# Kernel optimization log

Measured on AMD Instinct MI355X. Metric: run time of the kernel, lower is better.

Reference implementation:

```python
import jax, jax.numpy as jnp
import numpy as np

INPUT_DIM, CB_DIM, CB_VOCAB = 512, 16, 8192
N = 16384
EPS = 1e-12  # F.normalize default eps


def setup_inputs() -> dict:
    key = jax.random.key(0)
    kx, kp, kc = jax.random.split(key, 3)
    x = jax.random.normal(kx, (N, INPUT_DIM), dtype=jnp.float32)
    # xavier_uniform_ on P [input_dim, cb_dim]
    bound = float(np.sqrt(6.0 / (INPUT_DIM + CB_DIM)))
    P = jax.random.uniform(kp, (INPUT_DIM, CB_DIM), dtype=jnp.float32,
                           minval=-bound, maxval=bound)
    # CB = F.normalize(randn(cb_vocab, cb_dim)) -> unit rows
    CB = jax.random.normal(kc, (CB_VOCAB, CB_DIM), dtype=jnp.float32)
    CB = CB / jnp.maximum(jnp.linalg.norm(CB, axis=1, keepdims=True), EPS)
    return {"x": x, "P": P, "CB": CB}


def reference(x, P, CB):
    # random projection: [N, input_dim] @ [input_dim, cb_dim] -> [N, cb_dim]
    xp = x @ P
    # L2-normalize projected vectors (rows)
    xp = xp / jnp.maximum(jnp.linalg.norm(xp, axis=1, keepdims=True), EPS)
    # cosine similarity against unit-norm codebook = plain dot product
    sim = xp @ CB.T  # [N, cb_vocab]
    return jnp.argmax(sim, axis=1)  # [N] int codebook indices
```

## Files before the change

kernel.cpp:

```cpp
#include <hip/hip_runtime.h>
#include <stdint.h>

#define N_ROWS   16384
#define IN_DIM   512
#define CB_DIM   16
#define CB_VOCAB 8192

#define PROJ_ROWS 128
#define PROJ_GROUPS (N_ROWS / PROJ_ROWS)
#define KSPLIT 4
#define PROJ_BLOCKS (PROJ_GROUPS * KSPLIT)

#define N_RT   (N_ROWS / 16)
#define N_CT   (CB_VOCAB / 16)
#define CODEPARTS 16
#define CT_PER_PART (N_CT / CODEPARTS)

#define WS_OFF_XPP   0
#define WS_OFF_AFA   (4u << 20)
#define WS_OFF_AFB   (5u << 20)
#define WS_OFF_BHH   (6u << 20)
#define WS_OFF_B31   ((6u << 20) + (512u << 10))
#define WS_OFF_PART  (7u << 20)

typedef __attribute__((ext_vector_type(8))) short bf16x8;
typedef __attribute__((ext_vector_type(4))) float f32x4;

__device__ __forceinline__ unsigned fkey(float f) {
    unsigned u = __float_as_uint(f);
    return (u & 0x80000000u) ? ~u : (u | 0x80000000u);
}

__device__ __forceinline__ unsigned short f2bf(float f) {
    unsigned u = __float_as_uint(f);
    return (unsigned short)((u + 0x7FFFu + ((u >> 16) & 1u)) >> 16);
}
__device__ __forceinline__ float bf2f(unsigned short h) {
    return __uint_as_float(((unsigned)h) << 16);
}

__global__ __launch_bounds__(256, 4)
void k_front(const float* __restrict__ x, const float* __restrict__ P,
             const float* __restrict__ CB, float* __restrict__ xp_part,
             bf16x8* __restrict__ Bhh, bf16x8* __restrict__ B31) {
    __shared__ float4 Ps[128 * 4];
    __shared__ float  accs[4][128][17];

    const int wave = threadIdx.x >> 6;
    const int lane = threadIdx.x & 63;

    if (blockIdx.x >= PROJ_BLOCKS) {
        const int ct   = (blockIdx.x - PROJ_BLOCKS) * 4 + wave;
        const int n    = lane & 15;
        const int quad = lane >> 4;
        const int kh   = (quad & 1) * 8;
        const int lvl  = quad >> 1;
        const int code = ct * 16 + n;

        const float4* b4 = (const float4*)(CB + (size_t)code * CB_DIM + kh);
        float4 a = b4[0], b = b4[1];
        float v[8] = {a.x, a.y, a.z, a.w, b.x, b.y, b.z, b.w};

        bf16x8 shh, s31;
#pragma unroll
        for (int j = 0; j < 8; ++j) {
            float f = v[j];
            unsigned short b1 = f2bf(f);  float r1 = f - bf2f(b1);
            unsigned short b2 = f2bf(r1); float r2 = r1 - bf2f(b2);
            unsigned short b3 = f2bf(r2);
            shh[j] = (short)(lvl ? b2 : b1);
            s31[j] = (short)(lvl ? b1 : b3);
        }
        Bhh[(size_t)ct * 64 + lane] = shh;
        B31[(size_t)ct * 64 + lane] = s31;
        return;
    }

    const int g = blockIdx.x >> 2;
    const int p = blockIdx.x & 3;

    for (int i = threadIdx.x; i < 512; i += 256)
        Ps[i] = ((const float4*)P)[p * 512 + i];
    __syncthreads();

    const int row0 = PROJ_ROWS * g + 2 * lane;
    const int kabs = 128 * p + 32 * wave;

    float acc0[16], acc1[16];
#pragma unroll
    for (int c = 0; c < 16; ++c) { acc0[c] = 0.f; acc1[c] = 0.f; }

    const float4* xr0 = (const float4*)(x + (size_t)row0 * IN_DIM + kabs);
    const float4* xr1 = (const float4*)(x + (size_t)(row0 + 1) * IN_DIM + kabs);

#pragma unroll
    for (int i = 0; i < 8; ++i) {
        float4 xa = xr0[i];
        float4 xb = xr1[i];
        float xas[4] = {xa.x, xa.y, xa.z, xa.w};
        float xbs[4] = {xb.x, xb.y, xb.z, xb.w};
#pragma unroll
        for (int kk = 0; kk < 4; ++kk) {
#pragma unroll
            for (int q = 0; q < 4; ++q) {
                float4 pv = Ps[(32 * wave + 4 * i + kk) * 4 + q];
                acc0[4 * q + 0] += xas[kk] * pv.x;
                acc0[4 * q + 1] += xas[kk] * pv.y;
                acc0[4 * q + 2] += xas[kk] * pv.z;
                acc0[4 * q + 3] += xas[kk] * pv.w;
                acc1[4 * q + 0] += xbs[kk] * pv.x;
                acc1[4 * q + 1] += xbs[kk] * pv.y;
                acc1[4 * q + 2] += xbs[kk] * pv.z;
                acc1[4 * q + 3] += xbs[kk] * pv.w;
            }
        }
    }

#pragma unroll
    for (int c = 0; c < 16; ++c) {
        accs[wave][2 * lane][c]     = acc0[c];
        accs[wave][2 * lane + 1][c] = acc1[c];
    }
    __syncthreads();

    float4* xpp = (float4*)xp_part;
#pragma unroll
    for (int it = 0; it < 2; ++it) {
        int idx = threadIdx.x + 256 * it;
        int r = idx >> 2, q = idx & 3;
        float4 s = {0.f, 0.f, 0.f, 0.f};
#pragma unroll
        for (int w = 0; w < 4; ++w) {
            s.x += accs[w][r][4 * q + 0];
            s.y += accs[w][r][4 * q + 1];
            s.z += accs[w][r][4 * q + 2];
            s.w += accs[w][r][4 * q + 3];
        }
        xpp[(size_t)p * (N_ROWS * 4) + (size_t)(PROJ_ROWS * g + r) * 4 + q] = s;
    }
}

__global__ __launch_bounds__(256, 4)
void k_fold_frag(const float* __restrict__ xp_part,
                 bf16x8* __restrict__ AfragA, bf16x8* __restrict__ AfragB) {
    const int wave = threadIdx.x >> 6;
    const int lane = threadIdx.x & 63;
    const int rt   = blockIdx.x * 4 + wave;
    const int m    = lane & 15;
    const int quad = lane >> 4;
    const int kh   = (quad & 1) * 8;
    const int lvl  = quad >> 1;
    const int row  = rt * 16 + m;

    const float* base = xp_part + (size_t)row * 16 + kh;
    float4 u0 = {0.f,0.f,0.f,0.f}, u1 = {0.f,0.f,0.f,0.f};
#pragma unroll
    for (int p = 0; p < 4; ++p) {
        const float4* b4 = (const float4*)(base + (size_t)p * (N_ROWS * 16));
        float4 a = b4[0], b = b4[1];
        u0.x += a.x; u0.y += a.y; u0.z += a.z; u0.w += a.w;
        u1.x += b.x; u1.y += b.y; u1.z += b.z; u1.w += b.w;
    }
    float v[8] = {u0.x, u0.y, u0.z, u0.w, u1.x, u1.y, u1.z, u1.w};

    bf16x8 sa, sb;
#pragma unroll
    for (int j = 0; j < 8; ++j) {
        float f = v[j];
        unsigned short b1 = f2bf(f);  float r1 = f - bf2f(b1);
        unsigned short b2 = f2bf(r1); float r2 = r1 - bf2f(b2);
        unsigned short b3 = f2bf(r2);
        sa[j] = (short)(lvl ? b2 : b1);
        sb[j] = (short)(lvl ? b3 : b1);
    }
    AfragA[(size_t)rt * 64 + lane] = sa;
    AfragB[(size_t)rt * 64 + lane] = sb;
}

__global__ __launch_bounds__(256, 4)
void k_scan(const bf16x8* __restrict__ AfragA, const bf16x8* __restrict__ AfragB,
            const bf16x8* __restrict__ Bhh, const bf16x8* __restrict__ B31,
            unsigned long long* __restrict__ part) {
    const int codepart = blockIdx.x & (CODEPARTS - 1);
    const int rowgrp   = blockIdx.x >> 4;
    const int wave     = threadIdx.x >> 6;
    const int lane     = threadIdx.x & 63;
    const int n        = lane & 15;
    const int quad     = lane >> 4;
    const int rt_base  = rowgrp * 16 + wave * 4;

    bf16x8 Aa[4], Ab[4];
#pragma unroll
    for (int t = 0; t < 4; ++t) {
        Aa[t] = AfragA[(size_t)(rt_base + t) * 64 + lane];
        Ab[t] = AfragB[(size_t)(rt_base + t) * 64 + lane];
    }

    float bestv[4][4];
    int   bestc[4][4];
#pragma unroll
    for (int t = 0; t < 4; ++t)
#pragma unroll
        for (int r = 0; r < 4; ++r) { bestv[t][r] = -INFINITY; bestc[t][r] = 0; }

    const int ct0 = codepart * CT_PER_PART;
    size_t ib = (size_t)ct0 * 64;
    bf16x8 nb1  = Bhh[ib + lane];
    bf16x8 nb1s = Bhh[ib + (lane ^ 32)];
    bf16x8 nb3  = B31[ib + lane];

    for (int c = 0; c < CT_PER_PART; ++c) {
        bf16x8 b1 = nb1, b1s = nb1s, b3 = nb3;
        if (c + 1 < CT_PER_PART) {
            size_t ibn = (size_t)(ct0 + c + 1) * 64;
            nb1  = Bhh[ibn + lane];
            nb1s = Bhh[ibn + (lane ^ 32)];
            nb3  = B31[ibn + lane];
        }
#pragma unroll
        for (int t = 0; t < 4; ++t) {
            f32x4 s = __builtin_amdgcn_mfma_f32_16x16x32_bf16(
                          Aa[t], b1, (f32x4){0.f, 0.f, 0.f, 0.f}, 0, 0, 0);
            s = __builtin_amdgcn_mfma_f32_16x16x32_bf16(Aa[t], b1s, s, 0, 0, 0);
            s = __builtin_amdgcn_mfma_f32_16x16x32_bf16(Ab[t], b3,  s, 0, 0, 0);
#pragma unroll
            for (int r = 0; r < 4; ++r) {
                if (s[r] > bestv[t][r]) { bestv[t][r] = s[r]; bestc[t][r] = c; }
            }
        }
    }

#pragma unroll
    for (int t = 0; t < 4; ++t) {
#pragma unroll
        for (int r = 0; r < 4; ++r) {
            unsigned code = (unsigned)(codepart * 512 + bestc[t][r] * 16 + n);
            unsigned long long packed =
                ((unsigned long long)fkey(bestv[t][r]) << 32) |
                (unsigned long long)(0xFFFFFFFFu - code);
#pragma unroll
            for (int mk = 1; mk <= 8; mk <<= 1) {
                unsigned long long o = __shfl_xor(packed, mk, 64);
                packed = (o > packed) ? o : packed;
            }
            if (n == 0) {
                int row = (rt_base + t) * 16 + quad * 4 + r;
                part[(size_t)codepart * N_ROWS + row] = packed;
            }
        }
    }
}

__global__ __launch_bounds__(256, 4)
void k_reduce(const unsigned long long* __restrict__ part,
              int* __restrict__ out) {
    int row = blockIdx.x * 256 + threadIdx.x;
    unsigned long long best = 0ull;
#pragma unroll
    for (int c = 0; c < CODEPARTS; ++c) {
        unsigned long long v = part[(size_t)c * N_ROWS + row];
        best = (v > best) ? v : best;
    }
    out[row] = (int)(0xFFFFFFFFu - (unsigned)(best & 0xFFFFFFFFull));
}

extern "C" void kernel_launch(void* const* d_in, const int* in_sizes, int n_in,
                              void* d_out, int out_size, void* d_ws, size_t ws_size,
                              hipStream_t stream) {
    const float* x  = (const float*)d_in[0];
    const float* P  = (const float*)d_in[1];
    const float* CB = (const float*)d_in[2];
    int* out = (int*)d_out;

    char* ws = (char*)d_ws;
    float*  xp_part = (float*)(ws + WS_OFF_XPP);
    bf16x8* AfragA  = (bf16x8*)(ws + WS_OFF_AFA);
    bf16x8* AfragB  = (bf16x8*)(ws + WS_OFF_AFB);
    bf16x8* Bhh     = (bf16x8*)(ws + WS_OFF_BHH);
    bf16x8* B31     = (bf16x8*)(ws + WS_OFF_B31);
    unsigned long long* part = (unsigned long long*)(ws + WS_OFF_PART);

    k_front<<<PROJ_BLOCKS + N_CT / 4, 256, 0, stream>>>(x, P, CB, xp_part,
                                                        Bhh, B31);
    k_fold_frag<<<N_RT / 4, 256, 0, stream>>>(xp_part, AfragA, AfragB);
    k_scan<<<(N_RT / 16) * CODEPARTS, 256, 0, stream>>>(AfragA, AfragB,
                                                        Bhh, B31, part);
    k_reduce<<<N_ROWS / 256, 256, 0, stream>>>(part, out);
}
```

Baseline: 113.9 us.

## Fuse projection with fragment packing and fold argmax reduction into scan via atomics

The projection kernel now handles 32 full rows per block. It reduces the K-split partial sums in shared memory and emits the bf16 split fragments directly, which removes the separate fold kernel and the xp_part global round trip. The final argmax reduction kernel is also removed. The scan does a 64-bit atomicMax into a per-row slot, and the last block per row group, found with an atomic counter, writes the output indices. This cuts the launch count from four to two and drops the intermediate traffic, at the cost of atomic contention and lower occupancy in the front kernel (launch bounds go from 4 to 2).

Result: no change. 113.7 us (median of 2 runs) (-0.2%).

```diff
diff --git a/kernel.cpp b/kernel.cpp
--- a/kernel.cpp
+++ b/kernel.cpp
@@ -6,22 +6,21 @@
 #define CB_DIM   16
 #define CB_VOCAB 8192
 
-#define PROJ_ROWS 128
-#define PROJ_GROUPS (N_ROWS / PROJ_ROWS)
-#define KSPLIT 4
-#define PROJ_BLOCKS (PROJ_GROUPS * KSPLIT)
+#define PROJ_BLOCKS 512
+#define PREP_BLOCKS 128
 
 #define N_RT   (N_ROWS / 16)
 #define N_CT   (CB_VOCAB / 16)
 #define CODEPARTS 16
 #define CT_PER_PART (N_CT / CODEPARTS)
-
-#define WS_OFF_XPP   0
-#define WS_OFF_AFA   (4u << 20)
-#define WS_OFF_AFB   (5u << 20)
-#define WS_OFF_BHH   (6u << 20)
-#define WS_OFF_B31   ((6u << 20) + (512u << 10))
-#define WS_OFF_PART  (7u << 20)
+#define N_ROWGRP 64
+
+#define WS_OFF_AFA  0
+#define WS_OFF_AFB  (1u << 20)
+#define WS_OFF_BHH  (2u << 20)
+#define WS_OFF_B31  ((2u << 20) + (512u << 10))
+#define WS_OFF_PART (3u << 20)
+#define WS_OFF_CNT  ((3u << 20) + (128u << 10))
 
 typedef __attribute__((ext_vector_type(8))) short bf16x8;
 typedef __attribute__((ext_vector_type(4))) float f32x4;
@@ -39,18 +38,24 @@
     return __uint_as_float(((unsigned)h) << 16);
 }
 
-__global__ __launch_bounds__(256, 4)
+__global__ __launch_bounds__(256, 2)
 void k_front(const float* __restrict__ x, const float* __restrict__ P,
-             const float* __restrict__ CB, float* __restrict__ xp_part,
-             bf16x8* __restrict__ Bhh, bf16x8* __restrict__ B31) {
-    __shared__ float4 Ps[128 * 4];
-    __shared__ float  accs[4][128][17];
+             const float* __restrict__ CB,
+             bf16x8* __restrict__ AfragA, bf16x8* __restrict__ AfragB,
+             bf16x8* __restrict__ Bhh, bf16x8* __restrict__ B31,
+             unsigned long long* __restrict__ part, unsigned* __restrict__ cnt) {
+    __shared__ float4 Ps[IN_DIM * 4];
+    __shared__ float  accs[8][32][20];
 
     const int wave = threadIdx.x >> 6;
     const int lane = threadIdx.x & 63;
 
     if (blockIdx.x >= PROJ_BLOCKS) {
-        const int ct   = (blockIdx.x - PROJ_BLOCKS) * 4 + wave;
+        const int pb = blockIdx.x - PROJ_BLOCKS;
+        if (threadIdx.x < 128) part[pb * 128 + threadIdx.x] = 0ull;
+        if (pb == 0 && threadIdx.x < 64) cnt[threadIdx.x] = 0u;
+
+        const int ct   = pb * 4 + wave;
         const int n    = lane & 15;
         const int quad = lane >> 4;
         const int kh   = (quad & 1) * 8;
@@ -76,111 +81,83 @@
         return;
     }
 
-    const int g = blockIdx.x >> 2;
-    const int p = blockIdx.x & 3;
-
-    for (int i = threadIdx.x; i < 512; i += 256)
-        Ps[i] = ((const float4*)P)[p * 512 + i];
-    __syncthreads();
-
-    const int row0 = PROJ_ROWS * g + 2 * lane;
-    const int kabs = 128 * p + 32 * wave;
-
-    float acc0[16], acc1[16];
-#pragma unroll
-    for (int c = 0; c < 16; ++c) { acc0[c] = 0.f; acc1[c] = 0.f; }
-
-    const float4* xr0 = (const float4*)(x + (size_t)row0 * IN_DIM + kabs);
-    const float4* xr1 = (const float4*)(x + (size_t)(row0 + 1) * IN_DIM + kabs);
-
-#pragma unroll
-    for (int i = 0; i < 8; ++i) {
-        float4 xa = xr0[i];
-        float4 xb = xr1[i];
-        float xas[4] = {xa.x, xa.y, xa.z, xa.w};
-        float xbs[4] = {xb.x, xb.y, xb.z, xb.w};
+    const int b = blockIdx.x;
+    for (int i = threadIdx.x; i < IN_DIM * 4; i += 256)
+        Ps[i] = ((const float4*)P)[i];
+    __syncthreads();
+
+    const int r32   = lane & 31;
+    const int khalf = lane >> 5;
+    const int row   = b * 32 + r32;
+    const int kb    = 128 * wave + 64 * khalf;
+
+    float acc[16];
+#pragma unroll
+    for (int c = 0; c < 16; ++c) acc[c] = 0.0f;
+
+    const float4* xr = (const float4*)(x + (size_t)row * IN_DIM + kb);
+
+#pragma unroll 4
+    for (int i = 0; i < 16; ++i) {
+        float4 xv = xr[i];
+        float xs[4] = {xv.x, xv.y, xv.z, xv.w};
 #pragma unroll
         for (int kk = 0; kk < 4; ++kk) {
 #pragma unroll
             for (int q = 0; q < 4; ++q) {
-                float4 pv = Ps[(32 * wave + 4 * i + kk) * 4 + q];
-                acc0[4 * q + 0] += xas[kk] * pv.x;
-                acc0[4 * q + 1] += xas[kk] * pv.y;
-                acc0[4 * q + 2] += xas[kk] * pv.z;
-                acc0[4 * q + 3] += xas[kk] * pv.w;
-                acc1[4 * q + 0] += xbs[kk] * pv.x;
-                acc1[4 * q + 1] += xbs[kk] * pv.y;
-                acc1[4 * q + 2] += xbs[kk] * pv.z;
-                acc1[4 * q + 3] += xbs[kk] * pv.w;
-            }
-        }
-    }
-
-#pragma unroll
-    for (int c = 0; c < 16; ++c) {
-        accs[wave][2 * lane][c]     = acc0[c];
-        accs[wave][2 * lane + 1][c] = acc1[c];
-    }
-    __syncthreads();
-
-    float4* xpp = (float4*)xp_part;
-#pragma unroll
-    for (int it = 0; it < 2; ++it) {
-        int idx = threadIdx.x + 256 * it;
-        int r = idx >> 2, q = idx & 3;
-        float4 s = {0.f, 0.f, 0.f, 0.f};
-#pragma unroll
-        for (int w = 0; w < 4; ++w) {
-            s.x += accs[w][r][4 * q + 0];
-            s.y += accs[w][r][4 * q + 1];
-            s.z += accs[w][r][4 * q + 2];
-            s.w += accs[w][r][4 * q + 3];
-        }
-        xpp[(size_t)p * (N_ROWS * 4) + (size_t)(PROJ_ROWS * g + r) * 4 + q] = s;
-    }
-}
-
-__global__ __launch_bounds__(256, 4)
-void k_fold_frag(const float* __restrict__ xp_part,
-                 bf16x8* __restrict__ AfragA, bf16x8* __restrict__ AfragB) {
-    const int wave = threadIdx.x >> 6;
-    const int lane = threadIdx.x & 63;
-    const int rt   = blockIdx.x * 4 + wave;
-    const int m    = lane & 15;
-    const int quad = lane >> 4;
-    const int kh   = (quad & 1) * 8;
-    const int lvl  = quad >> 1;
-    const int row  = rt * 16 + m;
-
-    const float* base = xp_part + (size_t)row * 16 + kh;
-    float4 u0 = {0.f,0.f,0.f,0.f}, u1 = {0.f,0.f,0.f,0.f};
-#pragma unroll
-    for (int p = 0; p < 4; ++p) {
-        const float4* b4 = (const float4*)(base + (size_t)p * (N_ROWS * 16));
-        float4 a = b4[0], b = b4[1];
-        u0.x += a.x; u0.y += a.y; u0.z += a.z; u0.w += a.w;
-        u1.x += b.x; u1.y += b.y; u1.z += b.z; u1.w += b.w;
-    }
-    float v[8] = {u0.x, u0.y, u0.z, u0.w, u1.x, u1.y, u1.z, u1.w};
-
-    bf16x8 sa, sb;
-#pragma unroll
-    for (int j = 0; j < 8; ++j) {
-        float f = v[j];
-        unsigned short b1 = f2bf(f);  float r1 = f - bf2f(b1);
-        unsigned short b2 = f2bf(r1); float r2 = r1 - bf2f(b2);
-        unsigned short b3 = f2bf(r2);
-        sa[j] = (short)(lvl ? b2 : b1);
-        sb[j] = (short)(lvl ? b3 : b1);
-    }
-    AfragA[(size_t)rt * 64 + lane] = sa;
-    AfragB[(size_t)rt * 64 + lane] = sb;
+                float4 pv = Ps[(kb + 4 * i + kk) * 4 + q];
+                acc[4 * q + 0] += xs[kk] * pv.x;
+                acc[4 * q + 1] += xs[kk] * pv.y;
+                acc[4 * q + 2] += xs[kk] * pv.z;
+                acc[4 * q + 3] += xs[kk] * pv.w;
+            }
+        }
+    }
+
+    const int pslot = wave * 2 + khalf;
+#pragma unroll
+    for (int c = 0; c < 16; ++c) accs[pslot][r32][c] = acc[c];
+    __syncthreads();
+
+    if (threadIdx.x < 128) {
+        const int rtl  = threadIdx.x >> 6;
+        const int l2   = threadIdx.x & 63;
+        const int m    = l2 & 15;
+        const int quad = l2 >> 4;
+        const int kh   = (quad & 1) * 8;
+        const int lvl  = quad >> 1;
+        const int rloc = rtl * 16 + m;
+
+        float v[8];
+#pragma unroll
+        for (int j = 0; j < 8; ++j) v[j] = 0.0f;
+#pragma unroll
+        for (int p = 0; p < 8; ++p) {
+#pragma unroll
+            for (int j = 0; j < 8; ++j) v[j] += accs[p][rloc][kh + j];
+        }
+
+        bf16x8 sa, sb;
+#pragma unroll
+        for (int j = 0; j < 8; ++j) {
+            float f = v[j];
+            unsigned short b1 = f2bf(f);  float r1 = f - bf2f(b1);
+            unsigned short b2 = f2bf(r1); float r2 = r1 - bf2f(b2);
+            unsigned short b3 = f2bf(r2);
+            sa[j] = (short)(lvl ? b2 : b1);
+            sb[j] = (short)(lvl ? b3 : b1);
+        }
+        AfragA[(size_t)(2 * b + rtl) * 64 + l2] = sa;
+        AfragB[(size_t)(2 * b + rtl) * 64 + l2] = sb;
+    }
 }
 
 __global__ __launch_bounds__(256, 4)
 void k_scan(const bf16x8* __restrict__ AfragA, const bf16x8* __restrict__ AfragB,
             const bf16x8* __restrict__ Bhh, const bf16x8* __restrict__ B31,
-            unsigned long long* __restrict__ part) {
+            unsigned long long* __restrict__ part, unsigned* __restrict__ cnt,
+            int* __restrict__ out) {
+    __shared__ int s_done;
     const int codepart = blockIdx.x & (CODEPARTS - 1);
     const int rowgrp   = blockIdx.x >> 4;
     const int wave     = threadIdx.x >> 6;
@@ -245,23 +222,21 @@
             }
             if (n == 0) {
                 int row = (rt_base + t) * 16 + quad * 4 + r;
-                part[(size_t)codepart * N_ROWS + row] = packed;
-            }
-        }
-    }
-}
-
-__global__ __launch_bounds__(256, 4)
-void k_reduce(const unsigned long long* __restrict__ part,
-              int* __restrict__ out) {
-    int row = blockIdx.x * 256 + threadIdx.x;
-    unsigned long long best = 0ull;
-#pragma unroll
-    for (int c = 0; c < CODEPARTS; ++c) {
-        unsigned long long v = part[(size_t)c * N_ROWS + row];
-        best = (v > best) ? v : best;
-    }
-    out[row] = (int)(0xFFFFFFFFu - (unsigned)(best & 0xFFFFFFFFull));
+                atomicMax(&part[row], packed);
+            }
+        }
+    }
+
+    __syncthreads();
+    if (threadIdx.x == 0)
+        s_done = (atomicAdd(&cnt[rowgrp], 1u) == (unsigned)(CODEPARTS - 1));
+    __syncthreads();
+
+    if (s_done) {
+        int row = rowgrp * 256 + threadIdx.x;
+        unsigned long long v = atomicAdd(&part[row], 0ull);
+        out[row] = (int)(0xFFFFFFFFu - (unsigned)(v & 0xFFFFFFFFull));
+    }
 }
 
 extern "C" void kernel_launch(void* const* d_in, const int* in_sizes, int n_in,
@@ -273,17 +248,15 @@
     int* out = (int*)d_out;
 
     char* ws = (char*)d_ws;
-    float*  xp_part = (float*)(ws + WS_OFF_XPP);
-    bf16x8* AfragA  = (bf16x8*)(ws + WS_OFF_AFA);
-    bf16x8* AfragB  = (bf16x8*)(ws + WS_OFF_AFB);
-    bf16x8* Bhh     = (bf16x8*)(ws + WS_OFF_BHH);
-    bf16x8* B31     = (bf16x8*)(ws + WS_OFF_B31);
+    bf16x8* AfragA = (bf16x8*)(ws + WS_OFF_AFA);
+    bf16x8* AfragB = (bf16x8*)(ws + WS_OFF_AFB);
+    bf16x8* Bhh    = (bf16x8*)(ws + WS_OFF_BHH);
+    bf16x8* B31    = (bf16x8*)(ws + WS_OFF_B31);
     unsigned long long* part = (unsigned long long*)(ws + WS_OFF_PART);
-
-    k_front<<<PROJ_BLOCKS + N_CT / 4, 256, 0, stream>>>(x, P, CB, xp_part,
-                                                        Bhh, B31);
-    k_fold_frag<<<N_RT / 4, 256, 0, stream>>>(xp_part, AfragA, AfragB);
-    k_scan<<<(N_RT / 16) * CODEPARTS, 256, 0, stream>>>(AfragA, AfragB,
-                                                        Bhh, B31, part);
-    k_reduce<<<N_ROWS / 256, 256, 0, stream>>>(part, out);
-}
+    unsigned* cnt  = (unsigned*)(ws + WS_OFF_CNT);
+
+    k_front<<<PROJ_BLOCKS + PREP_BLOCKS, 256, 0, stream>>>(
+        x, P, CB, AfragA, AfragB, Bhh, B31, part, cnt);
+    k_scan<<<N_ROWGRP * CODEPARTS, 256, 0, stream>>>(
+        AfragA, AfragB, Bhh, B31, part, cnt, out);
+}
```

## Fuse argmax reduction into scan via atomicMax and last-block finalize

Applied to the files above, without the earlier changes.

Removes the separate reduce kernel by having each scan block atomicMax its packed (score, index) results into a single per-row slot, with a per-rowgroup counter so the last finishing block writes the final indices. The part buffer and counters are zeroed inside the front kernel's codebook-prep blocks. This saves a kernel launch and the 16-way partial write/read, at the cost of 64-bit global atomics and a last-block-done synchronization pattern.

Result: slower. 116.8 us (+2.6%).

```diff
diff --git a/kernel.cpp b/kernel.cpp
--- a/kernel.cpp
+++ b/kernel.cpp
@@ -10,18 +10,21 @@
 #define PROJ_GROUPS (N_ROWS / PROJ_ROWS)
 #define KSPLIT 4
 #define PROJ_BLOCKS (PROJ_GROUPS * KSPLIT)
+#define PREP_BLOCKS 128
 
 #define N_RT   (N_ROWS / 16)
 #define N_CT   (CB_VOCAB / 16)
 #define CODEPARTS 16
 #define CT_PER_PART (N_CT / CODEPARTS)
-
-#define WS_OFF_XPP   0
-#define WS_OFF_AFA   (4u << 20)
-#define WS_OFF_AFB   (5u << 20)
-#define WS_OFF_BHH   (6u << 20)
-#define WS_OFF_B31   ((6u << 20) + (512u << 10))
-#define WS_OFF_PART  (7u << 20)
+#define N_ROWGRP 64
+
+#define WS_OFF_XPP  0
+#define WS_OFF_AFA  (4u << 20)
+#define WS_OFF_AFB  (5u << 20)
+#define WS_OFF_BHH  (6u << 20)
+#define WS_OFF_B31  ((6u << 20) + (512u << 10))
+#define WS_OFF_PART (7u << 20)
+#define WS_OFF_CNT  ((7u << 20) + (128u << 10))
 
 typedef __attribute__((ext_vector_type(8))) short bf16x8;
 typedef __attribute__((ext_vector_type(4))) float f32x4;
@@ -42,7 +45,8 @@
 __global__ __launch_bounds__(256, 4)
 void k_front(const float* __restrict__ x, const float* __restrict__ P,
              const float* __restrict__ CB, float* __restrict__ xp_part,
-             bf16x8* __restrict__ Bhh, bf16x8* __restrict__ B31) {
+             bf16x8* __restrict__ Bhh, bf16x8* __restrict__ B31,
+             unsigned long long* __restrict__ part, unsigned* __restrict__ cnt) {
     __shared__ float4 Ps[128 * 4];
     __shared__ float  accs[4][128][17];
 
@@ -50,7 +54,11 @@
     const int lane = threadIdx.x & 63;
 
     if (blockIdx.x >= PROJ_BLOCKS) {
-        const int ct   = (blockIdx.x - PROJ_BLOCKS) * 4 + wave;
+        const int pb = blockIdx.x - PROJ_BLOCKS;
+        if (threadIdx.x < 128) part[pb * 128 + threadIdx.x] = 0ull;
+        if (pb == 0 && threadIdx.x < 64) cnt[threadIdx.x] = 0u;
+
+        const int ct   = pb * 4 + wave;
         const int n    = lane & 15;
         const int quad = lane >> 4;
         const int kh   = (quad & 1) * 8;
@@ -180,7 +188,9 @@
 __global__ __launch_bounds__(256, 4)
 void k_scan(const bf16x8* __restrict__ AfragA, const bf16x8* __restrict__ AfragB,
             const bf16x8* __restrict__ Bhh, const bf16x8* __restrict__ B31,
-            unsigned long long* __restrict__ part) {
+            unsigned long long* __restrict__ part, unsigned* __restrict__ cnt,
+            int* __restrict__ out) {
+    __shared__ int s_done;
     const int codepart = blockIdx.x & (CODEPARTS - 1);
     const int rowgrp   = blockIdx.x >> 4;
     const int wave     = threadIdx.x >> 6;
@@ -245,23 +255,21 @@
             }
             if (n == 0) {
                 int row = (rt_base + t) * 16 + quad * 4 + r;
-                part[(size_t)codepart * N_ROWS + row] = packed;
-            }
-        }
-    }
-}
-
-__global__ __launch_bounds__(256, 4)
-void k_reduce(const unsigned long long* __restrict__ part,
-              int* __restrict__ out) {
-    int row = blockIdx.x * 256 + threadIdx.x;
-    unsigned long long best = 0ull;
-#pragma unroll
-    for (int c = 0; c < CODEPARTS; ++c) {
-        unsigned long long v = part[(size_t)c * N_ROWS + row];
-        best = (v > best) ? v : best;
-    }
-    out[row] = (int)(0xFFFFFFFFu - (unsigned)(best & 0xFFFFFFFFull));
+                atomicMax(&part[row], packed);
+            }
+        }
+    }
+
+    __syncthreads();
+    if (threadIdx.x == 0)
+        s_done = (atomicAdd(&cnt[rowgrp], 1u) == (unsigned)(CODEPARTS - 1));
+    __syncthreads();
+
+    if (s_done) {
+        int row = rowgrp * 256 + threadIdx.x;
+        unsigned long long v = atomicAdd(&part[row], 0ull);
+        out[row] = (int)(0xFFFFFFFFu - (unsigned)(v & 0xFFFFFFFFull));
+    }
 }
 
 extern "C" void kernel_launch(void* const* d_in, const int* in_sizes, int n_in,
@@ -279,11 +287,11 @@
     bf16x8* Bhh     = (bf16x8*)(ws + WS_OFF_BHH);
     bf16x8* B31     = (bf16x8*)(ws + WS_OFF_B31);
     unsigned long long* part = (unsigned long long*)(ws + WS_OFF_PART);
-
-    k_front<<<PROJ_BLOCKS + N_CT / 4, 256, 0, stream>>>(x, P, CB, xp_part,
-                                                        Bhh, B31);
+    unsigned* cnt   = (unsigned*)(ws + WS_OFF_CNT);
+
+    k_front<<<PROJ_BLOCKS + PREP_BLOCKS, 256, 0, stream>>>(
+        x, P, CB, xp_part, Bhh, B31, part, cnt);
     k_fold_frag<<<N_RT / 4, 256, 0, stream>>>(xp_part, AfragA, AfragB);
-    k_scan<<<(N_RT / 16) * CODEPARTS, 256, 0, stream>>>(AfragA, AfragB,
-                                                        Bhh, B31, part);
-    k_reduce<<<N_ROWS / 256, 256, 0, stream>>>(part, out);
-}
+    k_scan<<<N_ROWGRP * CODEPARTS, 256, 0, stream>>>(
+        AfragA, AfragB, Bhh, B31, part, cnt, out);
+}
```
